# Kernel tuning notes

Hardware: AMD Instinct MI355X
Metric: run time of the kernel (lower is better)

The kernel has to match this reference:

```python
import jax, jax.numpy as jnp
import numpy as np
from jax import lax

V, K, XD, HD, ZD = 10000, 4, 256, 512, 128
N, T = 64, 256


def setup_inputs() -> dict:
    key = jax.random.key(0)
    ks = jax.random.split(key, 20)
    p = lambda k, shape: jax.random.normal(k, shape, jnp.float32) * 0.02
    return {
        "xs": jax.random.randint(ks[0], (N, T), 0, V),
        "ts": jax.random.randint(ks[1], (N, T), 0, V),
        "labels": jax.random.randint(ks[2], (N,), 0, K),
        "w": 1,
        "eps": jax.random.normal(ks[3], (N, T, ZD), jnp.float32),
        "h_noise": jax.random.uniform(ks[4], (N, HD), jnp.float32),
        "embed": p(ks[5], (V, XD)),
        "enc_w1": p(ks[6], (HD, XD + HD)), "enc_b1": jnp.zeros(HD),
        "enc_w2": p(ks[7], (HD, HD)), "enc_b2": jnp.zeros(HD),
        "enc_mean_w": p(ks[8], (ZD, HD)), "enc_mean_b": jnp.zeros(ZD),
        "enc_std_w": p(ks[9], (ZD, HD)), "enc_std_b": jnp.zeros(ZD),
        "dec_w1": p(ks[10], (HD, ZD + HD)), "dec_b1": jnp.zeros(HD),
        "dec_w2": p(ks[11], (HD, HD)), "dec_b2": jnp.zeros(HD),
        "dec_mean_w": p(ks[12], (XD, HD)), "dec_mean_b": jnp.zeros(XD),
        "gru_wih": p(ks[13], (3 * HD, XD + ZD)), "gru_whh": p(ks[14], (3 * HD, HD)),
        "gru_bih": jnp.zeros(3 * HD), "gru_bhh": jnp.zeros(3 * HD),
        "gen_w": p(ks[15], (V, XD)), "gen_b": jnp.zeros(V),
        "cls_w": p(ks[16], (K, HD)), "cls_b": jnp.zeros(K),
        "hinit_w": p(ks[17], (HD, 1)), "hinit_b": jnp.zeros(HD),
    }


def _lin(x, w, b):
    return x @ w.T + b


def _vrnn_losses(xs, ts, labels, w, eps, h_noise, embed,
                 enc_w1, enc_b1, enc_w2, enc_b2, enc_mean_w, enc_mean_b,
                 enc_std_w, enc_std_b, dec_w1, dec_b1, dec_w2, dec_b2,
                 dec_mean_w, dec_mean_b, gru_wih, gru_whh, gru_bih, gru_bhh,
                 gen_w, gen_b, cls_w, cls_b, hinit_w, hinit_b):
    # adaptive hidden init: Linear(1, h_dim) on float labels, plus uniform disturbance
    h0 = _lin(labels.astype(jnp.float32)[:, None], hinit_w, hinit_b)
    if w:
        h0 = h0 + h_noise
    x_emb = embed[xs]  # [N, T, XD]

    def step(h, inps):
        x_t, eps_t = inps  # [N, XD], [N, ZD]
        e = jax.nn.relu(_lin(jax.nn.relu(_lin(jnp.concatenate([x_t, h], 1), enc_w1, enc_b1)), enc_w2, enc_b2))
        mu = _lin(e, enc_mean_w, enc_mean_b)
        std = jax.nn.softplus(_lin(e, enc_std_w, enc_std_b))
        z = eps_t * std + mu  # reparameterized sample
        d = jax.nn.relu(_lin(jax.nn.relu(_lin(jnp.concatenate([z, h], 1), dec_w1, dec_b1)), dec_w2, dec_b2))
        dec_mean = jax.nn.sigmoid(_lin(d, dec_mean_w, dec_mean_b))  # [N, XD]
        # torch GRUCell
        gi = jnp.concatenate([x_t, z], 1) @ gru_wih.T + gru_bih
        gh = h @ gru_whh.T + gru_bhh
        ir, iz, in_ = jnp.split(gi, 3, axis=1)
        hr, hz, hn = jnp.split(gh, 3, axis=1)
        r = jax.nn.sigmoid(ir + hr)
        zg = jax.nn.sigmoid(iz + hz)
        n = jnp.tanh(in_ + r * hn)
        h_new = (1.0 - zg) * n + zg * h
        return h_new, dec_mean

    h_last, dec_means = lax.scan(step, h0, (x_emb.transpose(1, 0, 2), eps.transpose(1, 0, 2)))
    # dec_means: [T, N, XD] -> generation logits [T, N, V]
    logp = jax.nn.log_softmax(_lin(dec_means, gen_w, gen_b), axis=-1)
    gen_loss = -jnp.mean(jnp.take_along_axis(logp, ts.T[..., None], axis=-1))
    # classification on last hidden state (the dropout in the source is dead code)
    clogp = jax.nn.log_softmax(_lin(h_last, cls_w, cls_b), axis=-1)
    cla_loss = -jnp.mean(jnp.take_along_axis(clogp, labels[:, None], axis=-1))
    return gen_loss, cla_loss


def reference(xs, ts, labels, w, eps, h_noise, embed,
              enc_w1, enc_b1, enc_w2, enc_b2, enc_mean_w, enc_mean_b,
              enc_std_w, enc_std_b, dec_w1, dec_b1, dec_w2, dec_b2,
              dec_mean_w, dec_mean_b, gru_wih, gru_whh, gru_bih, gru_bhh,
              gen_w, gen_b, cls_w, cls_b, hinit_w, hinit_b):
    return _vrnn_losses(xs, ts, labels, w, eps, h_noise, embed,
                        enc_w1, enc_b1, enc_w2, enc_b2, enc_mean_w, enc_mean_b,
                        enc_std_w, enc_std_b, dec_w1, dec_b1, dec_w2, dec_b2,
                        dec_mean_w, dec_mean_b, gru_wih, gru_whh, gru_bih, gru_bhh,
                        gen_w, gen_b, cls_w, cls_b, hinit_w, hinit_b)
```

## Files before the change

### kernel.cpp

```cpp
#include <hip/hip_runtime.h>

typedef unsigned short u16;
typedef unsigned int u32;
typedef unsigned long long u64;
using bf16x8 = __attribute__((ext_vector_type(8))) short;
using f32x4  = __attribute__((ext_vector_type(4))) float;
using u32x4  = __attribute__((ext_vector_type(4))) unsigned int;

#define TT   256
#define NB   64
#define XDI  256
#define HDI  512
#define ZDI  128
#define VV   10000
#define RING 64
#define RMSK 63

#define OFF_WE1   512ull
#define OFF_WE2   786944ull
#define OFF_WMW   1311232ull
#define OFF_WSW   1442304ull
#define OFF_WD1   1573376ull
#define OFF_WD2   2228736ull
#define OFF_WDM   2753024ull
#define OFF_WIH   3015168ull
#define OFF_WHH   4194816ull
#define OFF_WGW   5767680ull
#define OFF_XEMB  10887680ull
#define OFF_H     19276288ull
#define OFF_ZALL  19997184ull
#define OFF_HALL  24191488ull
#define OFF_GPART 40968704ull
#define OFF_FLAG  41100800ull
#define OFF_GIX   41102848ull
#define OFF_C1X   91766784ull
#define OFF_C1A   108544000ull
#define OFF_EA    112738304ull

__device__ __forceinline__ u16 f2b(float f) {
  union { float f; u32 u; } v; v.f = f;
  u32 r = v.u + 0x7fffu + ((v.u >> 16) & 1u);
  return (u16)(r >> 16);
}
__device__ __forceinline__ u32 f2b2(float a, float b) {
  return (u32)f2b(a) | ((u32)f2b(b) << 16);
}
__device__ __forceinline__ float b2f(u16 x) {
  union { u32 u; float f; } v; v.u = ((u32)x) << 16; return v.f;
}

#define MFMA16(a, b, c) __builtin_amdgcn_mfma_f32_16x16x32_bf16(a, b, c, 0, 0, 0)

__device__ __forceinline__ const bf16x8* ldsB(const u16* base, int r, int K, int k) {
  return (const bf16x8*)((const char*)base + (((r * K + k) << 1) ^ ((r & 7) << 4)));
}
__device__ __forceinline__ void ldsW(u16* base, int r, int K, int k, uint4 v) {
  *(uint4*)((char*)base + (((r * K + k) << 1) ^ ((r & 7) << 4))) = v;
}

__device__ __forceinline__ void fill_lds(u16* lds, int Ktot,
                                         const u16* s0, int K0,
                                         const u16* s1, int K1) {
  int kch = Ktot >> 3;
  int nch = 64 * kch;
  for (int i = threadIdx.x; i < nch; i += 256) {
    int row = i / kch;
    int k = (i - row * kch) << 3;
    const u16* src = (k < K0) ? (s0 + row * K0 + k) : (s1 + row * K1 + (k - K0));
    uint4 v = *(const uint4*)src;
    ldsW(lds, row, Ktot, k, v);
  }
}

__device__ __forceinline__ void mm_tile(f32x4 acc[4], const u16* lds, int ldsStride, int ldsK0,
                                        const u16* __restrict__ W, int Kw, int wcol0,
                                        int Klen, int lane) {
  const int kl = (lane >> 4) << 3;
  const int cl = lane & 15;
  const u16* wp = W + (size_t)(wcol0 + cl) * Kw;
  for (int kc = 0; kc < Klen; kc += 32) {
    int k = kc + kl;
    bf16x8 b = *(const bf16x8*)(wp + k);
#pragma unroll
    for (int m = 0; m < 4; ++m)
      acc[m] = MFMA16(*ldsB(lds, (m << 4) + cl, ldsStride, ldsK0 + k), b, acc[m]);
  }
}

__device__ __forceinline__ void ld16_c(const void* p, u32x4* f) {
  asm volatile(
      "global_load_dwordx4 %0, %16, off sc0 sc1\n\t"
      "global_load_dwordx4 %1, %16, off offset:64 sc0 sc1\n\t"
      "global_load_dwordx4 %2, %16, off offset:128 sc0 sc1\n\t"
      "global_load_dwordx4 %3, %16, off offset:192 sc0 sc1\n\t"
      "global_load_dwordx4 %4, %16, off offset:256 sc0 sc1\n\t"
      "global_load_dwordx4 %5, %16, off offset:320 sc0 sc1\n\t"
      "global_load_dwordx4 %6, %16, off offset:384 sc0 sc1\n\t"
      "global_load_dwordx4 %7, %16, off offset:448 sc0 sc1\n\t"
      "global_load_dwordx4 %8, %16, off offset:512 sc0 sc1\n\t"
      "global_load_dwordx4 %9, %16, off offset:576 sc0 sc1\n\t"
      "global_load_dwordx4 %10, %16, off offset:640 sc0 sc1\n\t"
      "global_load_dwordx4 %11, %16, off offset:704 sc0 sc1\n\t"
      "global_load_dwordx4 %12, %16, off offset:768 sc0 sc1\n\t"
      "global_load_dwordx4 %13, %16, off offset:832 sc0 sc1\n\t"
      "global_load_dwordx4 %14, %16, off offset:896 sc0 sc1\n\t"
      "global_load_dwordx4 %15, %16, off offset:960 sc0 sc1\n\t"
      "s_waitcnt vmcnt(0)"
      : "=&v"(f[0]), "=&v"(f[1]), "=&v"(f[2]), "=&v"(f[3]),
        "=&v"(f[4]), "=&v"(f[5]), "=&v"(f[6]), "=&v"(f[7]),
        "=&v"(f[8]), "=&v"(f[9]), "=&v"(f[10]), "=&v"(f[11]),
        "=&v"(f[12]), "=&v"(f[13]), "=&v"(f[14]), "=&v"(f[15])
      : "v"(p) : "memory");
}
__device__ __forceinline__ void ld4_c(const void* p, u32x4* f) {
  asm volatile(
      "global_load_dwordx4 %0, %4, off sc0 sc1\n\t"
      "global_load_dwordx4 %1, %4, off offset:64 sc0 sc1\n\t"
      "global_load_dwordx4 %2, %4, off offset:128 sc0 sc1\n\t"
      "global_load_dwordx4 %3, %4, off offset:192 sc0 sc1\n\t"
      "s_waitcnt vmcnt(0)"
      : "=&v"(f[0]), "=&v"(f[1]), "=&v"(f[2]), "=&v"(f[3])
      : "v"(p) : "memory");
}
__device__ __forceinline__ void st16B_c(void* p, u32x4 v) {
  asm volatile("global_store_dwordx4 %0, %1, off sc0 sc1" :: "v"(p), "v"(v) : "memory");
}
__device__ __forceinline__ void st8B_c(void* p, u64 v) {
  asm volatile("global_store_dwordx2 %0, %1, off sc0 sc1" :: "v"(p), "v"(v) : "memory");
}
__device__ __forceinline__ void drain_vm() {
  asm volatile("s_waitcnt vmcnt(0)" ::: "memory");
}
__device__ __forceinline__ void postc(u32* cnt, int tid) {
  if (tid == 0)
    __hip_atomic_fetch_add(cnt, 1u, __ATOMIC_RELAXED, __HIP_MEMORY_SCOPE_AGENT);
}
__device__ __forceinline__ void pollc(u32* cnt, int tid, u32 target) {
  if (tid == 0) {
    while (__hip_atomic_load(cnt, __ATOMIC_RELAXED, __HIP_MEMORY_SCOPE_AGENT) < target)
      __builtin_amdgcn_s_sleep(1);
  }
  __syncthreads();
}
__device__ __forceinline__ f32x4 unpk4(u64 g) {
  f32x4 a;
#pragma unroll
  for (int j = 0; j < 4; ++j) a[j] = b2f((u16)(g >> (16 * j)));
  return a;
}
__device__ __forceinline__ float sigm(float x) { return 1.f / (1.f + __expf(-x)); }

struct ConvArgs { const float* s[10]; unsigned long long doff[10]; int n[10]; };

__global__ __launch_bounds__(256) void wconv(char* ws, ConvArgs a) {
  int seg = blockIdx.y;
  const float* s = a.s[seg];
  u16* d = (u16*)(ws + a.doff[seg]);
  int n = a.n[seg];
  int i = (blockIdx.x * 256 + threadIdx.x) * 8;
  if (i < n) {
    float4 v0 = *(const float4*)(s + i);
    float4 v1 = *(const float4*)(s + i + 4);
    uint4 o;
    o.x = f2b2(v0.x, v0.y); o.y = f2b2(v0.z, v0.w);
    o.z = f2b2(v1.x, v1.y); o.w = f2b2(v1.z, v1.w);
    *(uint4*)(d + i) = o;
  }
}

__global__ __launch_bounds__(256) void gatherx(char* ws, const int* xs, const float* embed) {
  u16* xemb = (u16*)(ws + OFF_XEMB);
  int i = blockIdx.x * 256 + threadIdx.x;
  int t = i >> 11;
  int rr = i & 2047;
  int n = rr >> 5;
  int k = (rr & 31) << 3;
  int idx = xs[n * TT + t];
  const float* src = embed + (size_t)idx * XDI + k;
  float4 v0 = *(const float4*)src;
  float4 v1 = *(const float4*)(src + 4);
  uint4 o;
  o.x = f2b2(v0.x, v0.y); o.y = f2b2(v0.z, v0.w);
  o.z = f2b2(v1.x, v1.y); o.w = f2b2(v1.z, v1.w);
  *(uint4*)(xemb + ((size_t)t * NB + n) * XDI + k) = o;
}

__global__ __launch_bounds__(256) void h0init(char* ws, const int* labels, const int* wflag,
                                              const float* hnoise, const float* hw, const float* hb0) {
  int i = blockIdx.x * 256 + threadIdx.x;
  int n = i >> 9, c = i & 511;
  float v = (float)labels[n] * hw[c] + hb0[c];
  if (wflag[0]) v += hnoise[i];
  ((float*)(ws + OFF_H))[i] = v;
  ((u16*)(ws + OFF_HALL))[i] = f2b(v);
}

__global__ __launch_bounds__(256) void gixk(char* ws, const float* bih, const float* b_e1) {
  __shared__ u16 lA[64 * 256];
  int t = blockIdx.x;
  int tid = threadIdx.x, wave = tid >> 6, lane = tid & 63;
  const int cl = lane & 15, rb = (lane >> 4) << 2;
  const u16* xemb = (const u16*)(ws + OFF_XEMB);
  const u16* wih = (const u16*)(ws + OFF_WIH);
  const u16* we1 = (const u16*)(ws + OFF_WE1);
  u16* gix = (u16*)(ws + OFF_GIX);
  u16* c1x = (u16*)(ws + OFF_C1X);
  fill_lds(lA, 256, xemb + (size_t)t * NB * XDI, 256, xemb, 256);
  __syncthreads();
  for (int ct = wave; ct < 128; ct += 4) {
    f32x4 acc[4];
    acc[0] = acc[1] = acc[2] = acc[3] = (f32x4){0.f, 0.f, 0.f, 0.f};
    if (ct < 96) {
      mm_tile(acc, lA, 256, 0, wih, 384, ct * 16, 256, lane);
      int col = ct * 16 + cl;
      float bv = bih[col];
      u16* dst = gix + ((size_t)t * 1536 + col) * 64;
#pragma unroll
      for (int m = 0; m < 4; ++m) {
        u64 o = (u64)f2b(acc[m][0] + bv) | ((u64)f2b(acc[m][1] + bv) << 16)
              | ((u64)f2b(acc[m][2] + bv) << 32) | ((u64)f2b(acc[m][3] + bv) << 48);
        *(u64*)(dst + (m << 4) + rb) = o;
      }
    } else {
      int c0 = (ct - 96) * 16;
      mm_tile(acc, lA, 256, 0, we1, 768, c0, 256, lane);
      int col = c0 + cl;
      float bv = b_e1[col];
      u16* dst = c1x + ((size_t)t * 512 + col) * 64;
#pragma unroll
      for (int m = 0; m < 4; ++m) {
        u64 o = (u64)f2b(acc[m][0] + bv) | ((u64)f2b(acc[m][1] + bv) << 16)
              | ((u64)f2b(acc[m][2] + bv) << 32) | ((u64)f2b(acc[m][3] + bv) << 48);
        *(u64*)(dst + (m << 4) + rb) = o;
      }
    }
  }
}

__global__ __launch_bounds__(256, 1) void phaseB(
    char* ws, const float* __restrict__ eps,
    const float* __restrict__ b_e2,
    const float* __restrict__ b_mw, const float* __restrict__ b_sw,
    const float* __restrict__ bhh) {
  __shared__ u16 wsl[59392];
  __shared__ float ghb[3][16][16];
  __shared__ float red[3][16][16];
  __shared__ float musp[16][8];
  __shared__ float hold[16][17];
  __shared__ __align__(16) u16 stg[16][16];

  u16* wWe1 = wsl;
  u16* wWhh = wsl + 12288;
  u16* wWe2 = wsl + 36864;
  u16* wWms = wsl + 45056;
  u16* wWihz = wsl + 53248;

  const u16* we1 = (const u16*)(ws + OFF_WE1);
  const u16* we2 = (const u16*)(ws + OFF_WE2);
  const u16* wmw = (const u16*)(ws + OFF_WMW);
  const u16* wsw = (const u16*)(ws + OFF_WSW);
  const u16* wih = (const u16*)(ws + OFF_WIH);
  const u16* whh = (const u16*)(ws + OFF_WHH);
  const u16* gix = (const u16*)(ws + OFF_GIX);
  const u16* c1x = (const u16*)(ws + OFF_C1X);
  float* hg = (float*)(ws + OFF_H);
  u16* zall = (u16*)(ws + OFF_ZALL);
  u16* hall = (u16*)(ws + OFF_HALL);

  const int tid = threadIdx.x, wave = tid >> 6, lane = tid & 63;
  const int cl = lane & 15, kl = (lane >> 4) << 3, rb = (lane >> 4) << 2;
  const int g = blockIdx.x >> 5, sl = blockIdx.x & 31;
  const int r0 = g << 4;

  u16* c1g = (u16*)(ws + OFF_C1A) + (size_t)g * (RING * 16 * 512);
  u16* eg  = (u16*)(ws + OFF_EA)  + (size_t)g * (RING * 16 * 512);
  u32* cC1 = (u32*)(ws + OFF_FLAG + (size_t)g * 1024);
  u32* cE  = (u32*)((char*)cC1 + 256);
  u32* cZ  = (u32*)((char*)cC1 + 512);
  u32* cH  = (u32*)((char*)cC1 + 768);

  for (int c = tid; c < 1536; c += 256) {
    int r = c / 96, k = (c % 96) << 3;
    ldsW(wWe1, r, 768, k, *(const uint4*)(we1 + (size_t)(sl * 16 + r) * 768 + k));
  }
  for (int c = tid; c < 3072; c += 256) {
    int r = c >> 6, k = (c & 63) << 3;
    int gr = (r >> 4) * 512 + sl * 16 + (r & 15);
    ldsW(wWhh, r, 512, k, *(const uint4*)(whh + (size_t)gr * 512 + k));
  }
  for (int c = tid; c < 1024; c += 256) {
    int r = c >> 6, k = (c & 63) << 3;
    ldsW(wWe2, r, 512, k, *(const uint4*)(we2 + (size_t)(sl * 16 + r) * 512 + k));
  }
  for (int c = tid; c < 1024; c += 256) {
    int r = c >> 6, k = (c & 63) << 3;
    uint4 v = {0, 0, 0, 0};
    if (r < 4)      v = *(const uint4*)(wmw + (size_t)(sl * 4 + r) * 512 + k);
    else if (r < 8) v = *(const uint4*)(wsw + (size_t)(sl * 4 + r - 4) * 512 + k);
    ldsW(wWms, r, 512, k, v);
  }
  for (int c = tid; c < 768; c += 256) {
    int r = c >> 4, k = (c & 15) << 3;
    int gr = (r >> 4) * 512 + sl * 16 + (r & 15);
    ldsW(wWihz, r, 128, k, *(const uint4*)(wih + (size_t)gr * 384 + 256 + k));
  }
  {
    int r = tid >> 4, c = tid & 15;
    hold[r][c] = hg[(size_t)(r0 + r) * 512 + sl * 16 + c];
  }
  const float be2 = b_e2[sl * 16 + cl];
  const float bms = (cl < 4) ? b_mw[sl * 4 + cl] : ((cl < 8) ? b_sw[sl * 4 + cl - 4] : 0.f);
  const float bhg = (wave >= 1) ? bhh[(wave - 1) * 512 + sl * 16 + cl] : 0.f;
  __syncthreads();

  const f32x4 z4 = {0.f, 0.f, 0.f, 0.f};
  for (int t = 0; t < TT; ++t) {
    const int rs = t & RMSK;
    u64 gx0 = 0, cx0 = 0;
    float4 ev4 = {0.f, 0.f, 0.f, 0.f};
    if (wave == 0)
      cx0 = *(const u64*)(c1x + ((size_t)t * 512 + sl * 16 + cl) * 64 + r0 + rb);
    if (wave < 3)
      gx0 = *(const u64*)(gix + ((size_t)t * 1536 + wave * 512 + sl * 16 + cl) * 64 + r0 + rb);
    if (wave == 0 && lane < 16)
      ev4 = *(const float4*)(eps + (size_t)(r0 + lane) * (TT * ZDI) + (size_t)t * ZDI + sl * 4);

    pollc(cH, tid, 32u * (u32)t);
    u32x4 hf[16];
    ld16_c(hall + ((size_t)t * NB + r0 + cl) * HDI + kl, hf);
    if (wave == 0) {
      f32x4 a = unpk4(cx0);
#pragma unroll
      for (int c = 0; c < 16; ++c)
        a = MFMA16(*(const bf16x8*)&hf[c], *ldsB(wWe1, cl, 768, 256 + c * 32 + kl), a);
#pragma unroll
      for (int j = 0; j < 4; ++j)
        stg[rb + j][cl] = f2b(fmaxf(a[j], 0.f));
      if (lane < 32) {
        int row = lane >> 1, half = lane & 1;
        u32x4 v = *(const u32x4*)&stg[row][half * 8];
        st16B_c(c1g + ((size_t)rs * 16 + row) * 512 + sl * 16 + half * 8, v);
      }
      drain_vm();
      postc(cC1, tid);
    } else {
      f32x4 a = z4;
#pragma unroll
      for (int c = 0; c < 16; ++c)
        a = MFMA16(*(const bf16x8*)&hf[c], *ldsB(wWhh, (wave - 1) * 16 + cl, 512, c * 32 + kl), a);
#pragma unroll
      for (int j = 0; j < 4; ++j) ghb[wave - 1][rb + j][cl] = a[j] + bhg;
    }

    pollc(cC1, tid, 32u * (u32)(t + 1));
    if (wave == 0) {
      u32x4 cf[16];
      ld16_c(c1g + ((size_t)rs * 16 + cl) * 512 + kl, cf);
      f32x4 a = z4;
#pragma unroll
      for (int c = 0; c < 16; ++c)
        a = MFMA16(*(const bf16x8*)&cf[c], *ldsB(wWe2, cl, 512, c * 32 + kl), a);
#pragma unroll
      for (int j = 0; j < 4; ++j)
        stg[rb + j][cl] = f2b(fmaxf(a[j] + be2, 0.f));
      if (lane < 32) {
        int row = lane >> 1, half = lane & 1;
        u32x4 v = *(const u32x4*)&stg[row][half * 8];
        st16B_c(eg + ((size_t)rs * 16 + row) * 512 + sl * 16 + half * 8, v);
      }
      drain_vm();
      postc(cE, tid);
    }

    pollc(cE, tid, 32u * (u32)(t + 1));
    if (wave == 0) {
      u32x4 ef[16];
      ld16_c(eg + ((size_t)rs * 16 + cl) * 512 + kl, ef);
      f32x4 a = z4;
#pragma unroll
      for (int c = 0; c < 16; ++c)
        a = MFMA16(*(const bf16x8*)&ef[c], *ldsB(wWms, cl, 512, c * 32 + kl), a);
      if (cl < 8) {
#pragma unroll
        for (int j = 0; j < 4; ++j) musp[rb + j][cl] = a[j] + bms;
      }
      if (lane < 16) {
        int r = lane;
        float m0 = musp[r][0], m1 = musp[r][1], m2 = musp[r][2], m3 = musp[r][3];
        float s0 = musp[r][4], s1 = musp[r][5], s2 = musp[r][6], s3 = musp[r][7];
        float p0 = fmaxf(s0, 0.f) + log1pf(__expf(-fabsf(s0)));
        float p1 = fmaxf(s1, 0.f) + log1pf(__expf(-fabsf(s1)));
        float p2 = fmaxf(s2, 0.f) + log1pf(__expf(-fabsf(s2)));
        float p3 = fmaxf(s3, 0.f) + log1pf(__expf(-fabsf(s3)));
        float z0 = ev4.x * p0 + m0, z1 = ev4.y * p1 + m1;
        float z2 = ev4.z * p2 + m2, z3 = ev4.w * p3 + m3;
        u64 pk = (u64)f2b2(z0, z1) | ((u64)f2b2(z2, z3) << 32);
        st8B_c(zall + ((size_t)t * NB + r0 + r) * ZDI + sl * 4, pk);
      }
      drain_vm();
      postc(cZ, tid);
    }

    pollc(cZ, tid, 32u * (u32)(t + 1));
    if (wave < 3) {
      u32x4 zf[4];
      ld4_c(zall + ((size_t)t * NB + r0 + cl) * ZDI + kl, zf);
      f32x4 a = unpk4(gx0);
#pragma unroll
      for (int c = 0; c < 4; ++c)
        a = MFMA16(*(const bf16x8*)&zf[c], *ldsB(wWihz, wave * 16 + cl, 128, c * 32 + kl), a);
#pragma unroll
      for (int j = 0; j < 4; ++j) red[wave][rb + j][cl] = a[j];
    }
    __syncthreads();
    {
      int r = tid >> 4, c = tid & 15;
      float rg = sigm(red[0][r][c] + ghb[0][r][c]);
      float zg = sigm(red[1][r][c] + ghb[1][r][c]);
      float ng = tanhf(red[2][r][c] + rg * ghb[2][r][c]);
      hold[r][c] = (1.f - zg) * ng + zg * hold[r][c];
    }
    __syncthreads();
    if (t < TT - 1) {
      if (wave == 0) {
        if (lane < 32) {
          int row = lane >> 1, half = lane & 1;
          const float* hp = &hold[row][half * 8];
          u32x4 w;
          w[0] = f2b2(hp[0], hp[1]); w[1] = f2b2(hp[2], hp[3]);
          w[2] = f2b2(hp[4], hp[5]); w[3] = f2b2(hp[6], hp[7]);
          st16B_c(hall + ((size_t)(t + 1) * NB + r0 + row) * HDI + sl * 16 + half * 8, w);
        }
        drain_vm();
        postc(cH, tid);
      }
    } else {
      int r = tid >> 4, c = tid & 15;
      hg[(size_t)(r0 + r) * 512 + sl * 16 + c] = hold[r][c];
    }
  }
}

__global__ __launch_bounds__(256, 1) void phaseC(
    char* ws, const float* db1, const float* db2, const float* dmbias,
    const float* genb, const int* ts, float* gpart) {
  __shared__ u16 lA[64 * 640];
  __shared__ u16 lB[64 * 512];
  int rb = blockIdx.x;
  int tid = threadIdx.x, wave = tid >> 6, lane = tid & 63;
  const u16* zall = (const u16*)(ws + OFF_ZALL);
  const u16* hall = (const u16*)(ws + OFF_HALL);
  const u16* wd1 = (const u16*)(ws + OFF_WD1);
  const u16* wd2 = (const u16*)(ws + OFF_WD2);
  const u16* wdm = (const u16*)(ws + OFF_WDM);
  const u16* wgw = (const u16*)(ws + OFF_WGW);

  fill_lds(lA, 640, zall + (size_t)rb * NB * ZDI, 128, hall + (size_t)rb * NB * HDI, 512);
  __syncthreads();
  for (int tile = wave; tile < 32; tile += 4) {
    f32x4 acc[4];
    acc[0] = acc[1] = acc[2] = acc[3] = (f32x4){0.f, 0.f, 0.f, 0.f};
    mm_tile(acc, lA, 640, 0, wd1, 640, tile * 16, 640, lane);
    int col = tile * 16 + (lane & 15);
    float bias = db1[col];
#pragma unroll
    for (int m = 0; m < 4; ++m)
#pragma unroll
      for (int j = 0; j < 4; ++j) {
        int row = (m << 4) + ((lane >> 4) << 2) + j;
        int byte = ((row * 512 + col) << 1) ^ ((row & 7) << 4);
        *(u16*)((char*)lB + byte) = f2b(fmaxf(acc[m][j] + bias, 0.f));
      }
  }
  __syncthreads();
  for (int tile = wave; tile < 32; tile += 4) {
    f32x4 acc[4];
    acc[0] = acc[1] = acc[2] = acc[3] = (f32x4){0.f, 0.f, 0.f, 0.f};
    mm_tile(acc, lB, 512, 0, wd2, 512, tile * 16, 512, lane);
    int col = tile * 16 + (lane & 15);
    float bias = db2[col];
#pragma unroll
    for (int m = 0; m < 4; ++m)
#pragma unroll
      for (int j = 0; j < 4; ++j) {
        int row = (m << 4) + ((lane >> 4) << 2) + j;
        int byte = ((row * 512 + col) << 1) ^ ((row & 7) << 4);
        *(u16*)((char*)lA + byte) = f2b(fmaxf(acc[m][j] + bias, 0.f));
      }
  }
  __syncthreads();
  for (int tile = wave; tile < 16; tile += 4) {
    f32x4 acc[4];
    acc[0] = acc[1] = acc[2] = acc[3] = (f32x4){0.f, 0.f, 0.f, 0.f};
    mm_tile(acc, lA, 512, 0, wdm, 512, tile * 16, 512, lane);
    int col = tile * 16 + (lane & 15);
    float bias = dmbias[col];
#pragma unroll
    for (int m = 0; m < 4; ++m)
#pragma unroll
      for (int j = 0; j < 4; ++j) {
        int row = (m << 4) + ((lane >> 4) << 2) + j;
        float v = 1.f / (1.f + __expf(-(acc[m][j] + bias)));
        int byte = ((row * 256 + col) << 1) ^ ((row & 7) << 4);
        *(u16*)((char*)lB + byte) = f2b(v);
      }
  }
  __syncthreads();
  float mr[16], sr[16], cap[16];
  int tg[16];
#pragma unroll
  for (int q = 0; q < 16; ++q) {
    int r = ((q >> 2) << 4) + ((lane >> 4) << 2) + (q & 3);
    tg[q] = ts[r * TT + rb];
    mr[q] = -1e30f; sr[q] = 0.f; cap[q] = -1e30f;
  }
  for (int ct = wave; ct < 625; ct += 4) {
    f32x4 acc[4];
    acc[0] = acc[1] = acc[2] = acc[3] = (f32x4){0.f, 0.f, 0.f, 0.f};
    mm_tile(acc, lB, 256, 0, wgw, 256, ct * 16, 256, lane);
    int colw = ct * 16 + (lane & 15);
    float gbv = genb[colw];
#pragma unroll
    for (int mi = 0; mi < 4; ++mi)
#pragma unroll
      for (int j = 0; j < 4; ++j) {
        int q = (mi << 2) + j;
        float v = acc[mi][j] + gbv;
        if (colw == tg[q]) cap[q] = v;
        float mn = fmaxf(mr[q], v);
        sr[q] = sr[q] * __expf(mr[q] - mn) + __expf(v - mn);
        mr[q] = mn;
      }
  }
#pragma unroll
  for (int d = 1; d < 16; d <<= 1) {
#pragma unroll
    for (int q = 0; q < 16; ++q) {
      float mo = __shfl_xor(mr[q], d);
      float so = __shfl_xor(sr[q], d);
      float co = __shfl_xor(cap[q], d);
      float mn = fmaxf(mr[q], mo);
      sr[q] = sr[q] * __expf(mr[q] - mn) + so * __expf(mo - mn);
      mr[q] = mn;
      cap[q] = fmaxf(cap[q], co);
    }
  }
  float* sc = (float*)lA;
  if ((lane & 15) == 0) {
    int gq = lane >> 4;
#pragma unroll
    for (int q = 0; q < 16; ++q) {
      int r = ((q >> 2) << 4) + (gq << 2) + (q & 3);
      sc[wave * 64 + r] = mr[q];
      sc[256 + wave * 64 + r] = sr[q];
      sc[512 + wave * 64 + r] = cap[q];
    }
  }
  __syncthreads();
  if (tid < 64) {
    float M = -1e30f, S = 0.f, C = -1e30f;
#pragma unroll
    for (int w = 0; w < 4; ++w) {
      float m = sc[w * 64 + tid], s = sc[256 + w * 64 + tid], c = sc[512 + w * 64 + tid];
      float mn = fmaxf(M, m);
      S = S * __expf(M - mn) + s * __expf(m - mn);
      M = mn;
      C = fmaxf(C, c);
    }
    float lossr = M + __logf(S) - C;
    for (int d = 1; d < 64; d <<= 1) lossr += __shfl_xor(lossr, d);
    if (tid == 0) gpart[rb] = lossr;
  }
}

__global__ __launch_bounds__(256) void finalk(char* ws, const int* labels,
                                              const float* cw, const float* cb,
                                              const float* gpart, float* out) {
  __shared__ float sred[256];
  __shared__ float cred[64];
  int tid = threadIdx.x;
  sred[tid] = gpart[tid];
  __syncthreads();
  for (int s2 = 128; s2 > 0; s2 >>= 1) {
    if (tid < s2) sred[tid] += sred[tid + s2];
    __syncthreads();
  }
  const float* h = (const float*)(ws + OFF_H);
  if (tid < 64) {
    const float* hrow = h + tid * 512;
    float a0 = cb[0], a1 = cb[1], a2 = cb[2], a3 = cb[3];
    for (int k = 0; k < 512; k += 4) {
      float4 hv = *(const float4*)(hrow + k);
      float4 w0 = *(const float4*)(cw + 0 * 512 + k);
      float4 w1 = *(const float4*)(cw + 1 * 512 + k);
      float4 w2 = *(const float4*)(cw + 2 * 512 + k);
      float4 w3 = *(const float4*)(cw + 3 * 512 + k);
      a0 += hv.x * w0.x + hv.y * w0.y + hv.z * w0.z + hv.w * w0.w;
      a1 += hv.x * w1.x + hv.y * w1.y + hv.z * w1.z + hv.w * w1.w;
      a2 += hv.x * w2.x + hv.y * w2.y + hv.z * w2.z + hv.w * w2.w;
      a3 += hv.x * w3.x + hv.y * w3.y + hv.z * w3.z + hv.w * w3.w;
    }
    float M = fmaxf(fmaxf(a0, a1), fmaxf(a2, a3));
    float S = __expf(a0 - M) + __expf(a1 - M) + __expf(a2 - M) + __expf(a3 - M);
    int lb = labels[tid];
    float lg = (lb == 0) ? a0 : (lb == 1) ? a1 : (lb == 2) ? a2 : a3;
    cred[tid] = M + __logf(S) - lg;
  }
  __syncthreads();
  if (tid == 0) {
    float cs = 0.f;
    for (int i = 0; i < 64; ++i) cs += cred[i];
    out[0] = sred[0] / 16384.f;
    out[1] = cs / 64.f;
  }
}

extern "C" void kernel_launch(void* const* d_in, const int* in_sizes, int n_in,
                              void* d_out, int out_size, void* d_ws, size_t ws_size,
                              hipStream_t stream) {
  (void)in_sizes; (void)n_in; (void)out_size; (void)ws_size;
  char* ws = (char*)d_ws;
  const int* xs = (const int*)d_in[0];
  const int* ts = (const int*)d_in[1];
  const int* labels = (const int*)d_in[2];
  const int* wflag = (const int*)d_in[3];
  const float* eps = (const float*)d_in[4];
  const float* hnoise = (const float*)d_in[5];
  const float* embed = (const float*)d_in[6];
  const float* e_w1 = (const float*)d_in[7];
  const float* e_b1 = (const float*)d_in[8];
  const float* e_w2 = (const float*)d_in[9];
  const float* e_b2 = (const float*)d_in[10];
  const float* m_w = (const float*)d_in[11];
  const float* m_b = (const float*)d_in[12];
  const float* s_w = (const float*)d_in[13];
  const float* s_b = (const float*)d_in[14];
  const float* d_w1 = (const float*)d_in[15];
  const float* d_b1 = (const float*)d_in[16];
  const float* d_w2 = (const float*)d_in[17];
  const float* d_b2 = (const float*)d_in[18];
  const float* dm_w = (const float*)d_in[19];
  const float* dm_b = (const float*)d_in[20];
  const float* g_ih = (const float*)d_in[21];
  const float* g_hh = (const float*)d_in[22];
  const float* g_bih = (const float*)d_in[23];
  const float* g_bhh = (const float*)d_in[24];
  const float* gw = (const float*)d_in[25];
  const float* gb = (const float*)d_in[26];
  const float* cw = (const float*)d_in[27];
  const float* cb = (const float*)d_in[28];
  const float* hw = (const float*)d_in[29];
  const float* hb0 = (const float*)d_in[30];

  hipMemsetAsync(ws + OFF_FLAG, 0, 4096, stream);

  ConvArgs ca;
  const float* srcs[10] = {e_w1, e_w2, m_w, s_w, d_w1, d_w2, dm_w, g_ih, g_hh, gw};
  unsigned long long doffs[10] = {OFF_WE1, OFF_WE2, OFF_WMW, OFF_WSW, OFF_WD1,
                                  OFF_WD2, OFF_WDM, OFF_WIH, OFF_WHH, OFF_WGW};
  int ns[10] = {393216, 262144, 65536, 65536, 327680, 262144, 131072, 589824, 786432, 2560000};
  for (int i = 0; i < 10; ++i) { ca.s[i] = srcs[i]; ca.doff[i] = doffs[i]; ca.n[i] = ns[i]; }

  wconv<<<dim3(1250, 10), 256, 0, stream>>>(ws, ca);
  gatherx<<<2048, 256, 0, stream>>>(ws, xs, embed);
  h0init<<<128, 256, 0, stream>>>(ws, labels, wflag, hnoise, hw, hb0);
  gixk<<<256, 256, 0, stream>>>(ws, g_bih, e_b1);
  phaseB<<<128, 256, 0, stream>>>(ws, eps, e_b2, m_b, s_b, g_bhh);
  phaseC<<<256, 256, 0, stream>>>(ws, d_b1, d_b2, dm_b, gb, ts, (float*)(ws + OFF_GPART));
  finalk<<<1, 256, 0, stream>>>(ws, labels, cw, cb, (const float*)(ws + OFF_GPART), (float*)d_out);
}
```

Measured before the change: 3.299 ms.

## Split recurrent phaseB batch into 8-row groups across 256 blocks

The recurrent phase now gives each block group 8 batch rows instead of 16, which doubles the grid to 256 blocks and the number of independent group-level flag chains. MFMA tiles stay 16 rows wide, so the upper half of each tile is redundant (rows are duplicated via crl) and its results are masked out. The intent is to spread the sequential per-timestep chain across more CUs to cut per-group latency. The cost is half-wasted MFMA work, twice the weight loads into LDS, and more flag traffic.

```diff
diff --git a/kernel.cpp b/kernel.cpp
--- a/kernel.cpp
+++ b/kernel.cpp
@@ -15,6 +15,8 @@
 #define VV   10000
 #define RING 64
 #define RMSK 63
+#define NCH  8
+#define CR   8
 
 #define OFF_WE1   512ull
 #define OFF_WE2   786944ull
@@ -243,11 +245,11 @@
     const float* __restrict__ b_mw, const float* __restrict__ b_sw,
     const float* __restrict__ bhh) {
   __shared__ u16 wsl[59392];
-  __shared__ float ghb[3][16][16];
-  __shared__ float red[3][16][16];
-  __shared__ float musp[16][8];
-  __shared__ float hold[16][17];
-  __shared__ __align__(16) u16 stg[16][16];
+  __shared__ float ghb[3][CR][16];
+  __shared__ float red[3][CR][16];
+  __shared__ float musp[CR][8];
+  __shared__ float hold[CR][17];
+  __shared__ __align__(16) u16 stg[CR][16];
 
   u16* wWe1 = wsl;
   u16* wWhh = wsl + 12288;
@@ -270,10 +272,11 @@
   const int tid = threadIdx.x, wave = tid >> 6, lane = tid & 63;
   const int cl = lane & 15, kl = (lane >> 4) << 3, rb = (lane >> 4) << 2;
   const int g = blockIdx.x >> 5, sl = blockIdx.x & 31;
-  const int r0 = g << 4;
-
-  u16* c1g = (u16*)(ws + OFF_C1A) + (size_t)g * (RING * 16 * 512);
-  u16* eg  = (u16*)(ws + OFF_EA)  + (size_t)g * (RING * 16 * 512);
+  const int r0 = g << 3;
+  const int crl = cl & 7;
+
+  u16* c1g = (u16*)(ws + OFF_C1A) + (size_t)g * (RING * CR * 512);
+  u16* eg  = (u16*)(ws + OFF_EA)  + (size_t)g * (RING * CR * 512);
   u32* cC1 = (u32*)(ws + OFF_FLAG + (size_t)g * 1024);
   u32* cE  = (u32*)((char*)cC1 + 256);
   u32* cZ  = (u32*)((char*)cC1 + 512);
@@ -304,7 +307,7 @@
     int gr = (r >> 4) * 512 + sl * 16 + (r & 15);
     ldsW(wWihz, r, 128, k, *(const uint4*)(wih + (size_t)gr * 384 + 256 + k));
   }
-  {
+  if (tid < CR * 16) {
     int r = tid >> 4, c = tid & 15;
     hold[r][c] = hg[(size_t)(r0 + r) * 512 + sl * 16 + c];
   }
@@ -319,27 +322,29 @@
     u64 gx0 = 0, cx0 = 0;
     float4 ev4 = {0.f, 0.f, 0.f, 0.f};
     if (wave == 0)
-      cx0 = *(const u64*)(c1x + ((size_t)t * 512 + sl * 16 + cl) * 64 + r0 + rb);
+      cx0 = *(const u64*)(c1x + ((size_t)t * 512 + sl * 16 + cl) * 64 + r0 + (rb & 7));
     if (wave < 3)
-      gx0 = *(const u64*)(gix + ((size_t)t * 1536 + wave * 512 + sl * 16 + cl) * 64 + r0 + rb);
-    if (wave == 0 && lane < 16)
+      gx0 = *(const u64*)(gix + ((size_t)t * 1536 + wave * 512 + sl * 16 + cl) * 64 + r0 + (rb & 7));
+    if (wave == 0 && lane < CR)
       ev4 = *(const float4*)(eps + (size_t)(r0 + lane) * (TT * ZDI) + (size_t)t * ZDI + sl * 4);
 
     pollc(cH, tid, 32u * (u32)t);
     u32x4 hf[16];
-    ld16_c(hall + ((size_t)t * NB + r0 + cl) * HDI + kl, hf);
+    ld16_c(hall + ((size_t)t * NB + r0 + crl) * HDI + kl, hf);
     if (wave == 0) {
       f32x4 a = unpk4(cx0);
 #pragma unroll
       for (int c = 0; c < 16; ++c)
         a = MFMA16(*(const bf16x8*)&hf[c], *ldsB(wWe1, cl, 768, 256 + c * 32 + kl), a);
-#pragma unroll
-      for (int j = 0; j < 4; ++j)
-        stg[rb + j][cl] = f2b(fmaxf(a[j], 0.f));
-      if (lane < 32) {
+      if (rb < CR) {
+#pragma unroll
+        for (int j = 0; j < 4; ++j)
+          stg[rb + j][cl] = f2b(fmaxf(a[j], 0.f));
+      }
+      if (lane < 16) {
         int row = lane >> 1, half = lane & 1;
         u32x4 v = *(const u32x4*)&stg[row][half * 8];
-        st16B_c(c1g + ((size_t)rs * 16 + row) * 512 + sl * 16 + half * 8, v);
+        st16B_c(c1g + ((size_t)rs * CR + row) * 512 + sl * 16 + half * 8, v);
       }
       drain_vm();
       postc(cC1, tid);
@@ -348,25 +353,29 @@
 #pragma unroll
       for (int c = 0; c < 16; ++c)
         a = MFMA16(*(const bf16x8*)&hf[c], *ldsB(wWhh, (wave - 1) * 16 + cl, 512, c * 32 + kl), a);
-#pragma unroll
-      for (int j = 0; j < 4; ++j) ghb[wave - 1][rb + j][cl] = a[j] + bhg;
+      if (rb < CR) {
+#pragma unroll
+        for (int j = 0; j < 4; ++j) ghb[wave - 1][rb + j][cl] = a[j] + bhg;
+      }
     }
 
     pollc(cC1, tid, 32u * (u32)(t + 1));
     if (wave == 0) {
       u32x4 cf[16];
-      ld16_c(c1g + ((size_t)rs * 16 + cl) * 512 + kl, cf);
+      ld16_c(c1g + ((size_t)rs * CR + crl) * 512 + kl, cf);
       f32x4 a = z4;
 #pragma unroll
       for (int c = 0; c < 16; ++c)
         a = MFMA16(*(const bf16x8*)&cf[c], *ldsB(wWe2, cl, 512, c * 32 + kl), a);
-#pragma unroll
-      for (int j = 0; j < 4; ++j)
-        stg[rb + j][cl] = f2b(fmaxf(a[j] + be2, 0.f));
-      if (lane < 32) {
+      if (rb < CR) {
+#pragma unroll
+        for (int j = 0; j < 4; ++j)
+          stg[rb + j][cl] = f2b(fmaxf(a[j] + be2, 0.f));
+      }
+      if (lane < 16) {
         int row = lane >> 1, half = lane & 1;
         u32x4 v = *(const u32x4*)&stg[row][half * 8];
-        st16B_c(eg + ((size_t)rs * 16 + row) * 512 + sl * 16 + half * 8, v);
+        st16B_c(eg + ((size_t)rs * CR + row) * 512 + sl * 16 + half * 8, v);
       }
       drain_vm();
       postc(cE, tid);
@@ -375,16 +384,16 @@
     pollc(cE, tid, 32u * (u32)(t + 1));
     if (wave == 0) {
       u32x4 ef[16];
-      ld16_c(eg + ((size_t)rs * 16 + cl) * 512 + kl, ef);
+      ld16_c(eg + ((size_t)rs * CR + crl) * 512 + kl, ef);
       f32x4 a = z4;
 #pragma unroll
       for (int c = 0; c < 16; ++c)
         a = MFMA16(*(const bf16x8*)&ef[c], *ldsB(wWms, cl, 512, c * 32 + kl), a);
-      if (cl < 8) {
+      if (rb < CR && cl < 8) {
 #pragma unroll
         for (int j = 0; j < 4; ++j) musp[rb + j][cl] = a[j] + bms;
       }
-      if (lane < 16) {
+      if (lane < CR) {
         int r = lane;
         float m0 = musp[r][0], m1 = musp[r][1], m2 = musp[r][2], m3 = musp[r][3];
         float s0 = musp[r][4], s1 = musp[r][5], s2 = musp[r][6], s3 = musp[r][7];
@@ -404,16 +413,18 @@
     pollc(cZ, tid, 32u * (u32)(t + 1));
     if (wave < 3) {
       u32x4 zf[4];
-      ld4_c(zall + ((size_t)t * NB + r0 + cl) * ZDI + kl, zf);
+      ld4_c(zall + ((size_t)t * NB + r0 + crl) * ZDI + kl, zf);
       f32x4 a = unpk4(gx0);
 #pragma unroll
       for (int c = 0; c < 4; ++c)
         a = MFMA16(*(const bf16x8*)&zf[c], *ldsB(wWihz, wave * 16 + cl, 128, c * 32 + kl), a);
-#pragma unroll
-      for (int j = 0; j < 4; ++j) red[wave][rb + j][cl] = a[j];
+      if (rb < CR) {
+#pragma unroll
+        for (int j = 0; j < 4; ++j) red[wave][rb + j][cl] = a[j];
+      }
     }
     __syncthreads();
-    {
+    if (tid < CR * 16) {
       int r = tid >> 4, c = tid & 15;
       float rg = sigm(red[0][r][c] + ghb[0][r][c]);
       float zg = sigm(red[1][r][c] + ghb[1][r][c]);
@@ -423,7 +434,7 @@
     __syncthreads();
     if (t < TT - 1) {
       if (wave == 0) {
-        if (lane < 32) {
+        if (lane < 16) {
           int row = lane >> 1, half = lane & 1;
           const float* hp = &hold[row][half * 8];
           u32x4 w;
@@ -435,8 +446,10 @@
         postc(cH, tid);
       }
     } else {
-      int r = tid >> 4, c = tid & 15;
-      hg[(size_t)(r0 + r) * 512 + sl * 16 + c] = hold[r][c];
+      if (tid < CR * 16) {
+        int r = tid >> 4, c = tid & 15;
+        hg[(size_t)(r0 + r) * 512 + sl * 16 + c] = hold[r][c];
+      }
     }
   }
 }
@@ -652,7 +665,7 @@
   const float* hw = (const float*)d_in[29];
   const float* hb0 = (const float*)d_in[30];
 
-  hipMemsetAsync(ws + OFF_FLAG, 0, 4096, stream);
+  hipMemsetAsync(ws + OFF_FLAG, 0, 8192, stream);
 
   ConvArgs ca;
   const float* srcs[10] = {e_w1, e_w2, m_w, s_w, d_w1, d_w2, dm_w, g_ih, g_hh, gw};
@@ -665,7 +678,7 @@
   gatherx<<<2048, 256, 0, stream>>>(ws, xs, embed);
   h0init<<<128, 256, 0, stream>>>(ws, labels, wflag, hnoise, hw, hb0);
   gixk<<<256, 256, 0, stream>>>(ws, g_bih, e_b1);
-  phaseB<<<128, 256, 0, stream>>>(ws, eps, e_b2, m_b, s_b, g_bhh);
+  phaseB<<<256, 256, 0, stream>>>(ws, eps, e_b2, m_b, s_b, g_bhh);
   phaseC<<<256, 256, 0, stream>>>(ws, d_b1, d_b2, dm_b, gb, ts, (float*)(ws + OFF_GPART));
   finalk<<<1, 256, 0, stream>>>(ws, labels, cw, cb, (const float*)(ws + OFF_GPART), (float*)d_out);
 }
```

Measured after the change: 3.162 ms. 1.04x faster.
